# Kernel tuning notes

Measured on AMD Instinct MI355X. Metric: run time of the kernel, lower is better.

The kernel has to match this reference:

```python
import jax, jax.numpy as jnp
import numpy as np

D = 1024   # embedding_dim
E = 8      # num_experts
H = 2048   # expert_hidden_dim
LN_EPS = 1e-5


def setup_inputs() -> dict:
    key = jax.random.key(0)
    ks = jax.random.split(key, 12)
    B, S = 4, 2048
    def lin_init(k, fan_in, shape):
        bound = 1.0 / np.sqrt(fan_in)
        return jax.random.uniform(k, shape, jnp.float32, -bound, bound)
    return {
        "input_tensor": jax.random.normal(ks[0], (B, S, D), jnp.float32),
        "expert_weights": jax.random.uniform(ks[1], (B, S, E), jnp.float32),
        "Wi": lin_init(ks[2], D, (D, H)),
        "bi": lin_init(ks[3], D, (H,)),
        "W1": lin_init(ks[4], H, (E, H, H)),
        "b1": lin_init(ks[5], H, (E, H)),
        "W2": lin_init(ks[6], H, (E, H, H)),
        "b2": lin_init(ks[7], H, (E, H)),
        "Wo": lin_init(ks[8], H, (H, D)),
        "bo": lin_init(ks[9], H, (D,)),
        "gamma": jnp.ones((D,), jnp.float32),
        "beta": jnp.zeros((D,), jnp.float32),
    }


def reference(input_tensor, expert_weights, Wi, bi, W1, b1, W2, b2, Wo, bo, gamma, beta):
    # shared input projection: [B,S,D] -> [B,S,H]
    h = jnp.einsum("bsd,dh->bsh", input_tensor, Wi) + bi
    # all-experts 2-layer MLP (dropout is identity in eval): [B,S,E,H]
    e1 = jax.nn.relu(jnp.einsum("bsh,ehk->bsek", h, W1) + b1)
    e2 = jax.nn.relu(jnp.einsum("bsek,ekj->bsej", e1, W2) + b2)
    # weighted combination over experts: [B,S,H]
    combined = jnp.einsum("bsej,bse->bsj", e2, expert_weights)
    # shared output projection: [B,S,D]
    out = jnp.einsum("bsh,hd->bsd", combined, Wo) + bo
    # layer norm over last dim
    mu = jnp.mean(out, axis=-1, keepdims=True)
    var = jnp.mean(jnp.square(out - mu), axis=-1, keepdims=True)
    return (out - mu) * jax.lax.rsqrt(var + LN_EPS) * gamma + beta
```

## Files before the change

kernel.cpp:

```cpp
#include <hip/hip_runtime.h>
#include <cstdint>
#include <cstddef>

__device__ __forceinline__ unsigned short f2h(float f) {
    union { _Float16 h; unsigned short u; } c; c.h = (_Float16)f; return c.u;
}
__device__ __forceinline__ float h2f(unsigned short u) {
    union { unsigned short u; _Float16 h; } c; c.u = u; return (float)c.h;
}

typedef _Float16 f16x8 __attribute__((ext_vector_type(8)));
typedef float    f32x4 __attribute__((ext_vector_type(4)));

__device__ __forceinline__ void gload16(const void* g, void* l) {
    __builtin_amdgcn_global_load_lds(
        (const __attribute__((address_space(1))) unsigned int*)g,
        (__attribute__((address_space(3))) unsigned int*)l,
        16, 0, 0);
}

#define BAR()   asm volatile("s_barrier" ::: "memory")
#define LGKM8() asm volatile("s_waitcnt lgkmcnt(8)" ::: "memory")
#define VMW(N)  asm volatile("s_waitcnt vmcnt(" #N ")" ::: "memory")
#define SETP(N) __builtin_amdgcn_s_setprio(N)

__global__ __launch_bounds__(256) void cvt_f32_f16(const float* __restrict__ in,
                                                   _Float16* __restrict__ out) {
    const size_t i = ((size_t)blockIdx.x * 256 + threadIdx.x) * 8;
    const float4 a = *(const float4*)(in + i);
    const float4 b = *(const float4*)(in + i + 4);
    f16x8 v;
    v[0] = (_Float16)a.x; v[1] = (_Float16)a.y; v[2] = (_Float16)a.z; v[3] = (_Float16)a.w;
    v[4] = (_Float16)b.x; v[5] = (_Float16)b.y; v[6] = (_Float16)b.z; v[7] = (_Float16)b.w;
    *(f16x8*)(out + i) = v;
}

__global__ __launch_bounds__(256) void transpose_cvt64(const float* __restrict__ in,
                                                       _Float16* __restrict__ out,
                                                       int R, int C) {
    __shared__ __align__(16) _Float16 tile[64][68];
    const int t = threadIdx.x;
    const int r0 = blockIdx.y << 6, c0 = blockIdx.x << 6;
#pragma unroll
    for (int p = 0; p < 4; ++p) {
        const int id  = p * 256 + t;
        const int row = id >> 4;
        const int cg  = (id & 15) << 2;
        const float4 v = *(const float4*)(in + (size_t)(r0 + row) * C + (c0 + cg));
        tile[cg + 0][row] = (_Float16)v.x;
        tile[cg + 1][row] = (_Float16)v.y;
        tile[cg + 2][row] = (_Float16)v.z;
        tile[cg + 3][row] = (_Float16)v.w;
    }
    __syncthreads();
#pragma unroll
    for (int p = 0; p < 4; ++p) {
        const int id   = p * 256 + t;
        const int crow = id >> 4;
        const int rg   = (id & 15) << 2;
        ushort4 v;
        v.x = ((const unsigned short*)&tile[crow][rg])[0];
        v.y = ((const unsigned short*)&tile[crow][rg])[1];
        v.z = ((const unsigned short*)&tile[crow][rg])[2];
        v.w = ((const unsigned short*)&tile[crow][rg])[3];
        *(ushort4*)((unsigned short*)out + (size_t)(c0 + crow) * R + (r0 + rg)) = v;
    }
}

__device__ __forceinline__ void mfma16(f32x4 (&acc)[4][2],
                                       const f16x8 (&a)[4][2],
                                       const f16x8 (&b)[2][2]) {
#pragma unroll
    for (int ks = 0; ks < 2; ++ks)
#pragma unroll
        for (int i = 0; i < 4; ++i)
#pragma unroll
            for (int j = 0; j < 2; ++j)
                acc[i][j] = __builtin_amdgcn_mfma_f32_16x16x32_f16(a[i][ks], b[j][ks], acc[i][j], 0, 0, 0);
}

template <int EPI>
__global__ __launch_bounds__(512, 2) void gemm256(
    const _Float16* __restrict__ A,
    const _Float16* __restrict__ BT,
    const float* __restrict__ bias,
    unsigned short* __restrict__ o16,
    float* __restrict__ of32,
    const float* __restrict__ ew,
    int M, int N, int K, int expert, int first)
{
    __shared__ __align__(16) _Float16 As[4 * 8192];
    __shared__ __align__(16) _Float16 Bs[4 * 8192];

    const int tid  = threadIdx.x;
    const int lane = tid & 63;
    const int wave = tid >> 6;
    const int quad = lane >> 4, r16 = lane & 15;
    const int wm = wave >> 2, wn = wave & 3;

    const int gx  = gridDim.x;
    const int nwg = gx * gridDim.y;
    int wg = blockIdx.y * gx + blockIdx.x;
    const int qch = nwg >> 3;
    wg = (wg & 7) * qch + (wg >> 3);
    const int m0 = (wg / gx) << 8;
    const int n0 = (wg % gx) << 8;

    const int nkt = K >> 6;

    const int srow  = tid >> 3;
    const int sslot = ((tid & 7) ^ (srow & 7)) << 3;
    const _Float16* gA = A  + (size_t)(m0 + srow) * K + sslot;
    const _Float16* gB = BT + (size_t)(n0 + srow) * K + sslot;
    _Float16* lA = As + tid * 8;
    _Float16* lB = Bs + tid * 8;
    const size_t rstep = (size_t)64 * K;
    const size_t hstep = (size_t)128 * K;

#define STAGE(gp, lp) do { gload16((gp), (lp)); gload16((gp) + rstep, (lp) + 4096); } while (0)

    const int s7   = r16 & 7;
    const int swk0 = (quad ^ s7) << 3;
    const int swk1 = ((quad + 4) ^ s7) << 3;
    const int rA   = (wm << 6) + r16;
    const int rB   = (wn << 5) + r16;
    const _Float16* aR0 = As + rA * 64 + swk0;
    const _Float16* aR1 = As + rA * 64 + swk1;
    const _Float16* bR0 = Bs + rB * 64 + swk0;
    const _Float16* bR1 = Bs + rB * 64 + swk1;

    f32x4 acc[2][2][4][2];
#pragma unroll
    for (int qm = 0; qm < 2; ++qm)
#pragma unroll
        for (int qn = 0; qn < 2; ++qn)
#pragma unroll
            for (int i = 0; i < 4; ++i)
#pragma unroll
                for (int j = 0; j < 2; ++j)
#pragma unroll
                    for (int r = 0; r < 4; ++r) acc[qm][qn][i][j][r] = 0.f;

    f16x8 af[4][2], bf0[2][2], bf1[2][2];

    STAGE(gA,             lA);
    STAGE(gB,             lB);
    STAGE(gB + hstep,     lB + 8192);
    STAGE(gA + hstep,     lA + 8192);
    VMW(4);
    STAGE(gA + 64,         lA + 16384);
    STAGE(gB + 64,         lB + 16384);
    STAGE(gB + 64 + hstep, lB + 24576);
    VMW(6);
    BAR();

#define TILE4(T, P)                                                            \
    {                                                                          \
        const int kc = (T) << 6;                                               \
                            \
        _Pragma("unroll")                                                      \
        for (int i = 0; i < 4; ++i) {                                          \
            af[i][0] = *(const f16x8*)(aR0 + (P)*16384 + i*1024);              \
            af[i][1] = *(const f16x8*)(aR1 + (P)*16384 + i*1024);              \
        }                                                                      \
        _Pragma("unroll")                                                      \
        for (int j = 0; j < 2; ++j) {                                          \
            bf0[j][0] = *(const f16x8*)(bR0 + (P)*16384 + j*1024);             \
            bf0[j][1] = *(const f16x8*)(bR1 + (P)*16384 + j*1024);             \
            bf1[j][0] = *(const f16x8*)(bR0 + (P)*16384 + 8192 + j*1024);      \
            bf1[j][1] = *(const f16x8*)(bR1 + (P)*16384 + 8192 + j*1024);      \
        }                                                                      \
        if ((T) + 1 < nkt) STAGE(gA + kc + 64 + hstep,                         \
                                 lA + ((1-(P))*2+1) * 8192);                   \
        LGKM8();                                                               \
        BAR();                                                                 \
        SETP(1); mfma16(acc[0][0], af, bf0); SETP(0);                          \
        BAR();                                                                 \
                             \
        if ((T) + 2 < nkt) STAGE(gA + kc + 128, lA + (P)*16384);               \
        BAR();                                                                 \
        SETP(1); mfma16(acc[0][1], af, bf1); SETP(0);                          \
        BAR();                                                                 \
                                    \
        _Pragma("unroll")                                                      \
        for (int i = 0; i < 4; ++i) {                                          \
            af[i][0] = *(const f16x8*)(aR0 + (P)*16384 + 8192 + i*1024);       \
            af[i][1] = *(const f16x8*)(aR1 + (P)*16384 + 8192 + i*1024);       \
        }                                                                      \
        if ((T) + 2 < nkt) STAGE(gB + kc + 128, lB + (P)*16384);               \
        BAR();                                                                 \
        SETP(1); mfma16(acc[1][0], af, bf0); SETP(0);                          \
        BAR();                                                                 \
                                                  \
        if ((T) + 2 < nkt) {                                                   \
            STAGE(gB + kc + 128 + hstep, lB + (P)*16384 + 8192);               \
            VMW(6);           \
        } else if ((T) + 1 < nkt) {                                            \
            VMW(0);            \
        }                                                                      \
        BAR();                                                                 \
        SETP(1); mfma16(acc[1][1], af, bf1); SETP(0);                          \
        BAR();                                                                 \
    }

    for (int t = 0; t < nkt; t += 2) {
        TILE4(t, 0)
        TILE4(t + 1, 1)
    }
#undef TILE4
#undef STAGE

    float bj[2][2];
#pragma unroll
    for (int qn = 0; qn < 2; ++qn)
#pragma unroll
        for (int j = 0; j < 2; ++j)
            bj[qn][j] = bias[n0 + qn * 128 + (wn << 5) + j * 16 + r16];

#pragma unroll
    for (int qm = 0; qm < 2; ++qm)
#pragma unroll
    for (int i = 0; i < 4; ++i) {
        const int mb = m0 + qm * 128 + (wm << 6) + i * 16 + (quad << 2);
#pragma unroll
        for (int r = 0; r < 4; ++r) {
            const int m = mb + r;
            float w = 0.f;
            if (EPI == 2) w = ew[(size_t)m * 8 + expert];
#pragma unroll
            for (int qn = 0; qn < 2; ++qn)
#pragma unroll
            for (int j = 0; j < 2; ++j) {
                const int n = n0 + qn * 128 + (wn << 5) + j * 16 + r16;
                const size_t idx = (size_t)m * N + n;
                float v = acc[qm][qn][i][j][r] + bj[qn][j];
                if (EPI == 0) {
                    o16[idx] = f2h(v);
                } else if (EPI == 1) {
                    o16[idx] = f2h(fmaxf(v, 0.f));
                } else if (EPI == 2) {
                    float tv = w * fmaxf(v, 0.f);
                    if (!first) tv += h2f(o16[idx]);
                    o16[idx] = f2h(tv);
                } else {
                    of32[idx] = v;
                }
            }
        }
    }
}

__global__ __launch_bounds__(256) void ln_rows(const float* __restrict__ x,
                                               const float* __restrict__ gamma,
                                               const float* __restrict__ beta,
                                               float* __restrict__ out) {
    const int row = blockIdx.x;
    const int t = threadIdx.x;
    const float4 v = *(const float4*)(x + (size_t)row * 1024 + t * 4);
    float s  = v.x + v.y + v.z + v.w;
    float ss = v.x * v.x + v.y * v.y + v.z * v.z + v.w * v.w;
#pragma unroll
    for (int off = 32; off > 0; off >>= 1) {
        s  += __shfl_down(s,  off, 64);
        ss += __shfl_down(ss, off, 64);
    }
    __shared__ float red[8];
    const int lane = t & 63, wv = t >> 6;
    if (lane == 0) { red[wv] = s; red[4 + wv] = ss; }
    __syncthreads();
    const float S  = red[0] + red[1] + red[2] + red[3];
    const float SS = red[4] + red[5] + red[6] + red[7];
    const float mean = S * (1.f / 1024.f);
    const float var  = SS * (1.f / 1024.f) - mean * mean;
    const float rstd = rsqrtf(var + 1e-5f);
    const float4 g4 = *(const float4*)(gamma + t * 4);
    const float4 b4 = *(const float4*)(beta + t * 4);
    float4 o;
    o.x = (v.x - mean) * rstd * g4.x + b4.x;
    o.y = (v.y - mean) * rstd * g4.y + b4.y;
    o.z = (v.z - mean) * rstd * g4.z + b4.z;
    o.w = (v.w - mean) * rstd * g4.w + b4.w;
    *(float4*)(out + (size_t)row * 1024 + t * 4) = o;
}

extern "C" void kernel_launch(void* const* d_in, const int* in_sizes, int n_in,
                              void* d_out, int out_size, void* d_ws, size_t ws_size,
                              hipStream_t stream) {
    const int M = 8192, D = 1024, H = 2048, E = 8;

    const float* X  = (const float*)d_in[0];
    const float* EW = (const float*)d_in[1];
    const float* Wi = (const float*)d_in[2];
    const float* bi = (const float*)d_in[3];
    const float* W1 = (const float*)d_in[4];
    const float* b1 = (const float*)d_in[5];
    const float* W2 = (const float*)d_in[6];
    const float* b2 = (const float*)d_in[7];
    const float* Wo = (const float*)d_in[8];
    const float* bo = (const float*)d_in[9];
    const float* gm = (const float*)d_in[10];
    const float* bt = (const float*)d_in[11];

    char* wsp = (char*)d_ws;
    size_t off = 0;
    auto alloc = [&](size_t bytes) { char* p = wsp + off; off += bytes; return p; };
    _Float16* WiT  = (_Float16*)alloc((size_t)H * D * 2);
    _Float16* WoT  = (_Float16*)alloc((size_t)D * H * 2);
    _Float16* W1Te = (_Float16*)alloc((size_t)H * H * 2);
    _Float16* W2Te = (_Float16*)alloc((size_t)H * H * 2);
    _Float16* Xh   = (_Float16*)alloc((size_t)M * D * 2);
    _Float16* h    = (_Float16*)alloc((size_t)M * H * 2);
    _Float16* e1   = (_Float16*)alloc((size_t)M * H * 2);
    _Float16* cmb  = (_Float16*)alloc((size_t)M * H * 2);
    float* preLN   = (float*)h;

    dim3 blk(256), gblk(512);

    cvt_f32_f16<<<(M * D) / 2048, blk, 0, stream>>>(X, Xh);
    transpose_cvt64<<<dim3(H / 64, D / 64), blk, 0, stream>>>(Wi, WiT, D, H);
    transpose_cvt64<<<dim3(D / 64, H / 64), blk, 0, stream>>>(Wo, WoT, H, D);

    gemm256<0><<<dim3(H / 256, M / 256), gblk, 0, stream>>>(
        Xh, WiT, bi, (unsigned short*)h, nullptr, nullptr, M, H, D, 0, 0);

    for (int e = 0; e < E; ++e) {
        transpose_cvt64<<<dim3(H / 64, H / 64), blk, 0, stream>>>(
            W1 + (size_t)e * H * H, W1Te, H, H);
        gemm256<1><<<dim3(H / 256, M / 256), gblk, 0, stream>>>(
            h, W1Te, b1 + (size_t)e * H, (unsigned short*)e1, nullptr, nullptr, M, H, H, 0, 0);
        transpose_cvt64<<<dim3(H / 64, H / 64), blk, 0, stream>>>(
            W2 + (size_t)e * H * H, W2Te, H, H);
        gemm256<2><<<dim3(H / 256, M / 256), gblk, 0, stream>>>(
            e1, W2Te, b2 + (size_t)e * H, (unsigned short*)cmb, nullptr, EW, M, H, H, e, e == 0);
    }

    gemm256<3><<<dim3(D / 256, M / 256), gblk, 0, stream>>>(
        cmb, WoT, bo, nullptr, preLN, nullptr, M, D, H, 0, 0);

    ln_rows<<<M, blk, 0, stream>>>(preLN, gm, bt, (float*)d_out);
}
```

Measured before the change: 1.734 ms.

## Prefetch next-tile MFMA fragments into registers and batch expert weight transposes

```diff
diff --git a/kernel.cpp b/kernel.cpp
--- a/kernel.cpp
+++ b/kernel.cpp
@@ -20,7 +20,6 @@
 }
 
 #define BAR()   asm volatile("s_barrier" ::: "memory")
-#define LGKM8() asm volatile("s_waitcnt lgkmcnt(8)" ::: "memory")
 #define VMW(N)  asm volatile("s_waitcnt vmcnt(" #N ")" ::: "memory")
 #define SETP(N) __builtin_amdgcn_s_setprio(N)
 
@@ -39,6 +38,7 @@
                                                        _Float16* __restrict__ out,
                                                        int R, int C) {
     __shared__ __align__(16) _Float16 tile[64][68];
+    const size_t zb = (size_t)blockIdx.z * R * C;
     const int t = threadIdx.x;
     const int r0 = blockIdx.y << 6, c0 = blockIdx.x << 6;
 #pragma unroll
@@ -46,7 +46,7 @@
         const int id  = p * 256 + t;
         const int row = id >> 4;
         const int cg  = (id & 15) << 2;
-        const float4 v = *(const float4*)(in + (size_t)(r0 + row) * C + (c0 + cg));
+        const float4 v = *(const float4*)(in + zb + (size_t)(r0 + row) * C + (c0 + cg));
         tile[cg + 0][row] = (_Float16)v.x;
         tile[cg + 1][row] = (_Float16)v.y;
         tile[cg + 2][row] = (_Float16)v.z;
@@ -63,7 +63,7 @@
         v.y = ((const unsigned short*)&tile[crow][rg])[1];
         v.z = ((const unsigned short*)&tile[crow][rg])[2];
         v.w = ((const unsigned short*)&tile[crow][rg])[3];
-        *(ushort4*)((unsigned short*)out + (size_t)(c0 + crow) * R + (r0 + rg)) = v;
+        *(ushort4*)((unsigned short*)out + zb + (size_t)(c0 + crow) * R + (r0 + rg)) = v;
     }
 }
 
@@ -154,60 +154,122 @@
     VMW(6);
     BAR();
 
+#pragma unroll
+    for (int i = 0; i < 4; ++i) {
+        af[i][0] = *(const f16x8*)(aR0 + i * 1024);
+        af[i][1] = *(const f16x8*)(aR1 + i * 1024);
+    }
+#pragma unroll
+    for (int j = 0; j < 2; ++j) {
+        bf0[j][0] = *(const f16x8*)(bR0 + j * 1024);
+        bf0[j][1] = *(const f16x8*)(bR1 + j * 1024);
+    }
+
 #define TILE4(T, P)                                                            \
     {                                                                          \
         const int kc = (T) << 6;                                               \
-                            \
-        _Pragma("unroll")                                                      \
-        for (int i = 0; i < 4; ++i) {                                          \
-            af[i][0] = *(const f16x8*)(aR0 + (P)*16384 + i*1024);              \
-            af[i][1] = *(const f16x8*)(aR1 + (P)*16384 + i*1024);              \
-        }                                                                      \
+                 \
         _Pragma("unroll")                                                      \
         for (int j = 0; j < 2; ++j) {                                          \
-            bf0[j][0] = *(const f16x8*)(bR0 + (P)*16384 + j*1024);             \
-            bf0[j][1] = *(const f16x8*)(bR1 + (P)*16384 + j*1024);             \
             bf1[j][0] = *(const f16x8*)(bR0 + (P)*16384 + 8192 + j*1024);      \
             bf1[j][1] = *(const f16x8*)(bR1 + (P)*16384 + 8192 + j*1024);      \
         }                                                                      \
         if ((T) + 1 < nkt) STAGE(gA + kc + 64 + hstep,                         \
                                  lA + ((1-(P))*2+1) * 8192);                   \
-        LGKM8();                                                               \
+        VMW(8);                            \
         BAR();                                                                 \
         SETP(1); mfma16(acc[0][0], af, bf0); SETP(0);                          \
         BAR();                                                                 \
+                                           \
+        if ((T) + 2 < nkt) STAGE(gA + kc + 128, lA + (P)*16384);               \
+        BAR();                                                                 \
+        SETP(1); mfma16(acc[0][1], af, bf1); SETP(0);                          \
+        BAR();                                                                 \
                              \
-        if ((T) + 2 < nkt) STAGE(gA + kc + 128, lA + (P)*16384);               \
-        BAR();                                                                 \
-        SETP(1); mfma16(acc[0][1], af, bf1); SETP(0);                          \
-        BAR();                                                                 \
-                                    \
         _Pragma("unroll")                                                      \
         for (int i = 0; i < 4; ++i) {                                          \
             af[i][0] = *(const f16x8*)(aR0 + (P)*16384 + 8192 + i*1024);       \
             af[i][1] = *(const f16x8*)(aR1 + (P)*16384 + 8192 + i*1024);       \
         }                                                                      \
         if ((T) + 2 < nkt) STAGE(gB + kc + 128, lB + (P)*16384);               \
+        if ((T) + 2 < nkt) { VMW(6); } else { VMW(0); }                        \
         BAR();                                                                 \
         SETP(1); mfma16(acc[1][0], af, bf0); SETP(0);                          \
         BAR();                                                                 \
-                                                  \
-        if ((T) + 2 < nkt) {                                                   \
-            STAGE(gB + kc + 128 + hstep, lB + (P)*16384 + 8192);               \
-            VMW(6);           \
-        } else if ((T) + 1 < nkt) {                                            \
-            VMW(0);            \
-        }                                                                      \
-        BAR();                                                                 \
-        SETP(1); mfma16(acc[1][1], af, bf1); SETP(0);                          \
+         \
+        if ((T) + 1 < nkt) {                                                   \
+            _Pragma("unroll")                                                  \
+            for (int i = 0; i < 4; ++i) {                                      \
+                af[i][0] = *(const f16x8*)(aR0 + (1-(P))*16384 + i*1024);      \
+                af[i][1] = *(const f16x8*)(aR1 + (1-(P))*16384 + i*1024);      \
+            }                                                                  \
+            _Pragma("unroll")                                                  \
+            for (int j = 0; j < 2; ++j) {                                      \
+                bf0[j][0] = *(const f16x8*)(bR0 + (1-(P))*16384 + j*1024);     \
+                bf0[j][1] = *(const f16x8*)(bR1 + (1-(P))*16384 + j*1024);     \
+            }                                                                  \
+        }                                                                      \
+        if ((T) + 2 < nkt) STAGE(gB + kc + 128 + hstep,                        \
+                                 lB + (P)*16384 + 8192);                       \
+        BAR();                                                                 \
+        SETP(1); mfma16(acc[1][1], afh1, bf1); SETP(0);                        \
+        BAR();                                                                 \
+    }
+
+    f16x8 afh1[4][2];
+#define TILE4B(T, P)                                                           \
+    {                                                                          \
+        const int kc = (T) << 6;                                               \
+        _Pragma("unroll")                                                      \
+        for (int j = 0; j < 2; ++j) {                                          \
+            bf1[j][0] = *(const f16x8*)(bR0 + (P)*16384 + 8192 + j*1024);      \
+            bf1[j][1] = *(const f16x8*)(bR1 + (P)*16384 + 8192 + j*1024);      \
+        }                                                                      \
+        if ((T) + 1 < nkt) STAGE(gA + kc + 64 + hstep,                         \
+                                 lA + ((1-(P))*2+1) * 8192);                   \
+        VMW(8);                                                                \
+        BAR();                                                                 \
+        SETP(1); mfma16(acc[0][0], af, bf0); SETP(0);                          \
+        BAR();                                                                 \
+        if ((T) + 2 < nkt) STAGE(gA + kc + 128, lA + (P)*16384);               \
+        BAR();                                                                 \
+        SETP(1); mfma16(acc[0][1], af, bf1); SETP(0);                          \
+        BAR();                                                                 \
+        _Pragma("unroll")                                                      \
+        for (int i = 0; i < 4; ++i) {                                          \
+            afh1[i][0] = *(const f16x8*)(aR0 + (P)*16384 + 8192 + i*1024);     \
+            afh1[i][1] = *(const f16x8*)(aR1 + (P)*16384 + 8192 + i*1024);     \
+        }                                                                      \
+        if ((T) + 2 < nkt) STAGE(gB + kc + 128, lB + (P)*16384);               \
+        if ((T) + 2 < nkt) { VMW(6); } else { VMW(0); }                        \
+        BAR();                                                                 \
+        SETP(1); mfma16(acc[1][0], afh1, bf0); SETP(0);                        \
+        BAR();                                                                 \
+        if ((T) + 1 < nkt) {                                                   \
+            _Pragma("unroll")                                                  \
+            for (int i = 0; i < 4; ++i) {                                      \
+                af[i][0] = *(const f16x8*)(aR0 + (1-(P))*16384 + i*1024);      \
+                af[i][1] = *(const f16x8*)(aR1 + (1-(P))*16384 + i*1024);      \
+            }                                                                  \
+            _Pragma("unroll")                                                  \
+            for (int j = 0; j < 2; ++j) {                                      \
+                bf0[j][0] = *(const f16x8*)(bR0 + (1-(P))*16384 + j*1024);     \
+                bf0[j][1] = *(const f16x8*)(bR1 + (1-(P))*16384 + j*1024);     \
+            }                                                                  \
+        }                                                                      \
+        if ((T) + 2 < nkt) STAGE(gB + kc + 128 + hstep,                        \
+                                 lB + (P)*16384 + 8192);                       \
+        BAR();                                                                 \
+        SETP(1); mfma16(acc[1][1], afh1, bf1); SETP(0);                        \
         BAR();                                                                 \
     }
 
     for (int t = 0; t < nkt; t += 2) {
-        TILE4(t, 0)
-        TILE4(t + 1, 1)
+        TILE4B(t, 0)
+        TILE4B(t + 1, 1)
     }
 #undef TILE4
+#undef TILE4B
 #undef STAGE
 
     float bj[2][2];
@@ -306,32 +368,45 @@
     auto alloc = [&](size_t bytes) { char* p = wsp + off; off += bytes; return p; };
     _Float16* WiT  = (_Float16*)alloc((size_t)H * D * 2);
     _Float16* WoT  = (_Float16*)alloc((size_t)D * H * 2);
-    _Float16* W1Te = (_Float16*)alloc((size_t)H * H * 2);
-    _Float16* W2Te = (_Float16*)alloc((size_t)H * H * 2);
     _Float16* Xh   = (_Float16*)alloc((size_t)M * D * 2);
     _Float16* h    = (_Float16*)alloc((size_t)M * H * 2);
     _Float16* e1   = (_Float16*)alloc((size_t)M * H * 2);
     _Float16* cmb  = (_Float16*)alloc((size_t)M * H * 2);
     float* preLN   = (float*)h;
 
+    const size_t perexp = (size_t)H * H * 2;
+    const bool big = (ws_size - off) >= 16 * perexp;
+    _Float16* W1T = (_Float16*)alloc(big ? 8 * perexp : perexp);
+    _Float16* W2T = (_Float16*)alloc(big ? 8 * perexp : perexp);
+
     dim3 blk(256), gblk(512);
 
     cvt_f32_f16<<<(M * D) / 2048, blk, 0, stream>>>(X, Xh);
-    transpose_cvt64<<<dim3(H / 64, D / 64), blk, 0, stream>>>(Wi, WiT, D, H);
-    transpose_cvt64<<<dim3(D / 64, H / 64), blk, 0, stream>>>(Wo, WoT, H, D);
+    transpose_cvt64<<<dim3(H / 64, D / 64, 1), blk, 0, stream>>>(Wi, WiT, D, H);
+    transpose_cvt64<<<dim3(D / 64, H / 64, 1), blk, 0, stream>>>(Wo, WoT, H, D);
+    if (big) {
+        transpose_cvt64<<<dim3(H / 64, H / 64, 8), blk, 0, stream>>>(W1, W1T, H, H);
+        transpose_cvt64<<<dim3(H / 64, H / 64, 8), blk, 0, stream>>>(W2, W2T, H, H);
+    }
 
     gemm256<0><<<dim3(H / 256, M / 256), gblk, 0, stream>>>(
         Xh, WiT, bi, (unsigned short*)h, nullptr, nullptr, M, H, D, 0, 0);
 
     for (int e = 0; e < E; ++e) {
-        transpose_cvt64<<<dim3(H / 64, H / 64), blk, 0, stream>>>(
-            W1 + (size_t)e * H * H, W1Te, H, H);
+        _Float16* w1t = big ? W1T + (size_t)e * H * H : W1T;
+        _Float16* w2t = big ? W2T + (size_t)e * H * H : W2T;
+        if (!big) {
+            transpose_cvt64<<<dim3(H / 64, H / 64, 1), blk, 0, stream>>>(
+                W1 + (size_t)e * H * H, w1t, H, H);
+        }
         gemm256<1><<<dim3(H / 256, M / 256), gblk, 0, stream>>>(
-            h, W1Te, b1 + (size_t)e * H, (unsigned short*)e1, nullptr, nullptr, M, H, H, 0, 0);
-        transpose_cvt64<<<dim3(H / 64, H / 64), blk, 0, stream>>>(
-            W2 + (size_t)e * H * H, W2Te, H, H);
+            h, w1t, b1 + (size_t)e * H, (unsigned short*)e1, nullptr, nullptr, M, H, H, 0, 0);
+        if (!big) {
+            transpose_cvt64<<<dim3(H / 64, H / 64, 1), blk, 0, stream>>>(
+                W2 + (size_t)e * H * H, w2t, H, H);
+        }
         gemm256<2><<<dim3(H / 256, M / 256), gblk, 0, stream>>>(
-            e1, W2Te, b2 + (size_t)e * H, (unsigned short*)cmb, nullptr, EW, M, H, H, e, e == 0);
+            e1, w2t, b2 + (size_t)e * H, (unsigned short*)cmb, nullptr, EW, M, H, H, e, e == 0);
     }
 
     gemm256<3><<<dim3(D / 256, M / 256), gblk, 0, stream>>>(
```

Measured after the change: 2.443 ms. 40.9% more time.
